# Kernel tuning notes

Hardware: AMD Instinct MI355X
Metric: run time of the kernel (lower is better)

The kernel has to match this reference:

```python
import jax, jax.numpy as jnp
import numpy as np

HID, SD, EXP, DTR = 1024, 16, 2048, 64
B_, T_ = 4, 2048


def setup_inputs() -> dict:
    key = jax.random.key(0)
    ks = jax.random.split(key, 9)
    def rn(k, shape, s=0.02):
        return jax.random.normal(k, shape, jnp.float32) * s
    return {
        "x": jax.random.normal(ks[0], (B_, T_, HID), jnp.float32),
        "ln_g": jnp.ones((HID,), jnp.float32),
        "ln_b": jnp.zeros((HID,), jnp.float32),
        "W_in": rn(ks[1], (HID, 2 * EXP)),
        "b_in": jnp.zeros((2 * EXP,), jnp.float32),
        "W_del": rn(ks[2], (EXP, DTR)),
        "b_del": jnp.zeros((DTR,), jnp.float32),
        "W_dt": rn(ks[3], (DTR, EXP)),
        "b_dt": jnp.zeros((EXP,), jnp.float32),
        "W_B": rn(ks[4], (EXP, SD)),
        "b_B": jnp.zeros((SD,), jnp.float32),
        "W_C": rn(ks[5], (EXP, SD)),
        "b_C": jnp.zeros((SD,), jnp.float32),
        "A_log": -jnp.exp(0.1 * jax.random.normal(ks[6], (EXP, SD), jnp.float32)),
        "Dp": jnp.zeros((EXP,), jnp.float32),
        "W_out": rn(ks[7], (EXP, HID)),
        "b_out": jnp.zeros((HID,), jnp.float32),
    }


def _layernorm(x, g, b, eps=1e-5):
    m = jnp.mean(x, axis=-1, keepdims=True)
    v = jnp.var(x, axis=-1, keepdims=True)
    return (x - m) * jax.lax.rsqrt(v + eps) * g + b


def _selective_scan(u, delta, A, Bm, Cm):
    # u, delta: (B,T,E); Bm, Cm: (B,T,Sd); A: (E,Sd)
    def step(h, inp):
        u_t, d_t, B_t, C_t = inp  # (B,E),(B,E),(B,Sd),(B,Sd)
        A_disc = jnp.exp(d_t[..., None] * A[None])          # (B,E,Sd)
        h = A_disc * h + d_t[..., None] * B_t[:, None, :] * u_t[..., None]
        y_t = jnp.einsum("bs,bds->bd", C_t, h)
        return h, y_t
    h0 = jnp.zeros((u.shape[0], u.shape[2], A.shape[1]), u.dtype)
    xs = (u.transpose(1, 0, 2), delta.transpose(1, 0, 2),
          Bm.transpose(1, 0, 2), Cm.transpose(1, 0, 2))
    _, ys = jax.lax.scan(step, h0, xs)  # ys: (T,B,E)
    return ys.transpose(1, 0, 2)


def reference(x, ln_g, ln_b, W_in, b_in, W_del, b_del, W_dt, b_dt,
              W_B, b_B, W_C, b_C, A_log, Dp, W_out, b_out):
    res = x
    xn = _layernorm(x, ln_g, ln_b)
    xp = xn @ W_in + b_in                 # (B,T,2E)
    u, gate = jnp.split(xp, 2, axis=-1)   # each (B,T,E)
    u = jax.nn.silu(u)
    delta = jax.nn.softplus((u @ W_del + b_del) @ W_dt + b_dt)  # (B,T,E)
    Bm = u @ W_B + b_B                    # (B,T,Sd)
    Cm = u @ W_C + b_C                    # (B,T,Sd)
    A = -jnp.exp(A_log)                   # (E,Sd)
    y = _selective_scan(u, delta, A, Bm, Cm)
    y = y + u * Dp
    y = y * jax.nn.silu(gate)
    return y @ W_out + b_out + res
```

## Files before the change

kernel.cpp:

```cpp
#include <hip/hip_runtime.h>

#define HIDN 1024
#define EXPN 2048
#define SDIM 16
#define DTRN 64
#define BBN  4
#define TTN  2048
#define MMN  (BBN*TTN)
#define NCHUNK 32
#define CLEN (TTN/NCHUNK)
#define KSPL 8
#define KCH  (EXPN/KSPL)

typedef unsigned short u16;
typedef __bf16 bf16x8 __attribute__((ext_vector_type(8)));
typedef float f32x4 __attribute__((ext_vector_type(4)));

static __device__ __forceinline__ float b2f(u16 u) {
    union { unsigned int i; float f; } cv; cv.i = ((unsigned int)u) << 16; return cv.f;
}
static __device__ __forceinline__ u16 f2b(float f) {
    union { float f; unsigned int i; } cv; cv.f = f;
    unsigned int x = cv.i;
    return (u16)((x + 0x7fffu + ((x >> 16) & 1u)) >> 16);
}
static __device__ __forceinline__ float fexp2(float x) {
    return __builtin_amdgcn_exp2f(x);
}
static __device__ __forceinline__ float fsilu(float v) {
    return v / (1.f + fexp2(-1.44269504088896f * v));
}
template<int L> static __device__ __forceinline__ void waitcnt_vm() {
    if constexpr (L == 0) asm volatile("s_waitcnt vmcnt(0)" ::: "memory");
    else if constexpr (L == 3) asm volatile("s_waitcnt vmcnt(3)" ::: "memory");
    else if constexpr (L == 4) asm volatile("s_waitcnt vmcnt(4)" ::: "memory");
}

static __device__ __forceinline__
void tr_tile(const float* __restrict__ W, u16* __restrict__ Wt,
             int K, int N, int bk, int bn, float (*t)[65]) {
    const int r0 = threadIdx.x >> 4, c0 = (threadIdx.x & 15) << 2;
    #pragma unroll
    for (int i = 0; i < 4; ++i) {
        float4 v = *(const float4*)(W + (size_t)(bk + r0 + i * 16) * N + bn + c0);
        t[r0 + i * 16][c0 + 0] = v.x; t[r0 + i * 16][c0 + 1] = v.y;
        t[r0 + i * 16][c0 + 2] = v.z; t[r0 + i * 16][c0 + 3] = v.w;
    }
    __syncthreads();
    #pragma unroll
    for (int i = 0; i < 4; ++i) {
        const int n = r0 + i * 16;
        ushort4 o;
        o.x = f2b(t[c0 + 0][n]); o.y = f2b(t[c0 + 1][n]);
        o.z = f2b(t[c0 + 2][n]); o.w = f2b(t[c0 + 3][n]);
        *(ushort4*)(Wt + (size_t)(bn + n) * K + bk + c0) = o;
    }
}

__global__ __launch_bounds__(256)
void k_prep(const float* __restrict__ x, const float* __restrict__ ln_g,
            const float* __restrict__ ln_b,
            const float* __restrict__ W_in, const float* __restrict__ W_out,
            const float* __restrict__ W_dt, const float* __restrict__ W_del,
            const float* __restrict__ W_B, const float* __restrict__ W_C,
            const float* __restrict__ A_log,
            u16* __restrict__ xn,
            u16* __restrict__ Wt_in, u16* __restrict__ Wt_out,
            u16* __restrict__ Wdt_t, u16* __restrict__ Wcat,
            float* __restrict__ A2) {
    __shared__ float t[64][65];
    __shared__ float as[4], bs[4];
    int blk = blockIdx.x;
    if (blk < MMN) {
        const int row = blk, tid = threadIdx.x;
        const float4 xv = ((const float4*)(x + (size_t)row * HIDN))[tid];
        float s  = xv.x + xv.y + xv.z + xv.w;
        float ss = fmaf(xv.x, xv.x, fmaf(xv.y, xv.y, fmaf(xv.z, xv.z, xv.w * xv.w)));
        #pragma unroll
        for (int o = 32; o > 0; o >>= 1) { s += __shfl_down(s, o); ss += __shfl_down(ss, o); }
        const int wid = tid >> 6, lane = tid & 63;
        if (lane == 0) { as[wid] = s; bs[wid] = ss; }
        __syncthreads();
        const float S  = as[0] + as[1] + as[2] + as[3];
        const float SS = bs[0] + bs[1] + bs[2] + bs[3];
        const float mean = S * (1.f / HIDN);
        const float var  = SS * (1.f / HIDN) - mean * mean;
        const float r = rsqrtf(var + 1e-5f);
        const float4 gv = ((const float4*)ln_g)[tid];
        const float4 bv = ((const float4*)ln_b)[tid];
        ushort4 o;
        o.x = f2b((xv.x - mean) * r * gv.x + bv.x);
        o.y = f2b((xv.y - mean) * r * gv.y + bv.y);
        o.z = f2b((xv.z - mean) * r * gv.z + bv.z);
        o.w = f2b((xv.w - mean) * r * gv.w + bv.w);
        ((ushort4*)(xn + (size_t)row * HIDN))[tid] = o;
        return;
    }
    blk -= MMN;
    if (blk < 1024) {
        tr_tile(W_in, Wt_in, HIDN, 2 * EXPN, (blk >> 6) << 6, (blk & 63) << 6, t);
        return;
    }
    blk -= 1024;
    if (blk < 512) {
        tr_tile(W_out, Wt_out, EXPN, HIDN, (blk >> 4) << 6, (blk & 15) << 6, t);
        return;
    }
    blk -= 512;
    if (blk < 32) {
        tr_tile(W_dt, Wdt_t, DTRN, EXPN, 0, blk << 6, t);
        return;
    }
    blk -= 32;
    if (blk < 768) {
        const int i = blk * 256 + threadIdx.x;
        const int n = i >> 11, k = i & 2047;
        float v;
        if (n < 64)      v = W_del[(size_t)k * DTRN + n];
        else if (n < 80) v = W_B[(size_t)k * SDIM + (n - 64)];
        else             v = W_C[(size_t)k * SDIM + (n - 80)];
        Wcat[i] = f2b(v);
        return;
    }
    blk -= 768;
    {
        const int i = blk * 256 + threadIdx.x;
        A2[i] = -__expf(A_log[i]) * 1.44269504088896340736f;
    }
}

#define MEPI_SPLIT_SILU 0
#define MEPI_OUT        1
#define MEPI_SP         2

template<int BN>
static __device__ __forceinline__
void stage256(const u16* __restrict__ A, const u16* __restrict__ Bt,
              u16 (*seg)[8192], int brow, int bcol, int K, int k0,
              int srow, int scol, int tid) {
    #pragma unroll
    for (int h = 0; h < 2; ++h) {
        const u16* sa = A + (size_t)(brow + h * 128 + srow) * K + k0 + scol;
        __builtin_amdgcn_global_load_lds(
            (const __attribute__((address_space(1))) void*)sa,
            (__attribute__((address_space(3))) void*)&seg[h][tid * 8], 16, 0, 0);
    }
    #pragma unroll
    for (int h = 0; h < BN / 128; ++h) {
        const u16* sb = Bt + (size_t)(bcol + h * 128 + srow) * K + k0 + scol;
        __builtin_amdgcn_global_load_lds(
            (const __attribute__((address_space(1))) void*)sb,
            (__attribute__((address_space(3))) void*)&seg[2 + h][tid * 8], 16, 0, 0);
    }
}

template<int BN, int EPI>
__global__ __launch_bounds__(1024)
void mgemm256(const u16* __restrict__ A, const u16* __restrict__ Bt,
              const float* __restrict__ bias, void* __restrict__ O0,
              void* __restrict__ O1, const float* __restrict__ res,
              int N, int K) {
    constexpr int NSEG = 2 + BN / 128;
    constexpr int L    = NSEG;
    constexpr int NF   = BN / 64 / 4 * 4 / 4;
    constexpr int NFRag = BN / 64;
    __shared__ u16 lds[2][NSEG][8192];
    const int tid  = threadIdx.x;
    const int lane = tid & 63, wid = tid >> 6;
    const int wm = wid >> 2, wn = wid & 3;
    const int r  = lane & 15, kh = lane >> 4;
    const int brow = blockIdx.y * 256, bcol = blockIdx.x * BN;

    int srow, scol;
    {
        const int q = tid;
        const int sub = q >> 6, qi = q & 63;
        const int qis = qi ^ (((qi >> 5) & 1) << 1);
        srow = (sub >> 1) * 16 + (qi >> 2);
        scol = ((sub & 1) << 5) + (qis & 3) * 8;
    }
    const int swz_kh = kh ^ (((r >> 3) & 1) << 1);
    const int rbase  = r * 32 + swz_kh * 8;
    const int am = wm & 1;

    f32x4 acc[4][NFRag];
    #pragma unroll
    for (int i = 0; i < 4; ++i)
        #pragma unroll
        for (int n = 0; n < NFRag; ++n) acc[i][n] = (f32x4){0.f, 0.f, 0.f, 0.f};

    const int NT = K >> 6;
    stage256<BN>(A, Bt, lds[0], brow, bcol, K, 0, srow, scol, tid);
    if (NT > 1) {
        stage256<BN>(A, Bt, lds[1], brow, bcol, K, 64, srow, scol, tid);
        waitcnt_vm<L>();
    } else {
        waitcnt_vm<0>();
    }
    __builtin_amdgcn_s_barrier();
    asm volatile("" ::: "memory");

    for (int kt = 0; kt < NT; ++kt) {
        const u16* segA = lds[kt & 1][wm >> 1];
        #pragma unroll
        for (int kk = 0; kk < 2; ++kk) {
            bf16x8 a[4], b[NFRag];
            #pragma unroll
            for (int mf = 0; mf < 4; ++mf)
                a[mf] = *(const bf16x8*)&segA[((am * 4 + mf) * 2 + kk) * 512 + rbase];
            #pragma unroll
            for (int nf = 0; nf < NFRag; ++nf) {
                const int nb = wn * NFRag + nf;
                const u16* segB = lds[kt & 1][2 + (nb >> 3)];
                b[nf] = *(const bf16x8*)&segB[(((nb & 7)) * 2 + kk) * 512 + rbase];
            }
            __builtin_amdgcn_s_setprio(1);
            #pragma unroll
            for (int mf = 0; mf < 4; ++mf)
                #pragma unroll
                for (int nf = 0; nf < NFRag; ++nf)
                    acc[mf][nf] = __builtin_amdgcn_mfma_f32_16x16x32_bf16(a[mf], b[nf], acc[mf][nf], 0, 0, 0);
            __builtin_amdgcn_s_setprio(0);
        }
        __builtin_amdgcn_s_barrier(); asm volatile("" ::: "memory");
        if (kt + 2 < NT) {
            stage256<BN>(A, Bt, lds[kt & 1], brow, bcol, K, (kt + 2) * 64, srow, scol, tid);
            waitcnt_vm<L>();
        } else {
            waitcnt_vm<0>();
        }
        __builtin_amdgcn_s_barrier(); asm volatile("" ::: "memory");
    }

    const int orow = brow + wm * 64 + kh * 4;
    const int ocol = bcol + wn * (BN / 4) + r;
    if constexpr (EPI == MEPI_SPLIT_SILU) {
        u16* dst; int cb;
        if (bcol < EXPN) { dst = (u16*)O0; cb = ocol; }
        else             { dst = (u16*)O1; cb = ocol - EXPN; }
        #pragma unroll
        for (int Mf = 0; Mf < 4; ++Mf)
            #pragma unroll
            for (int Nf = 0; Nf < NFRag; ++Nf)
                #pragma unroll
                for (int j = 0; j < 4; ++j) {
                    const int row = orow + Mf * 16 + j;
                    const int col = ocol + Nf * 16;
                    float v = acc[Mf][Nf][j] + bias[col];
                    dst[(size_t)row * EXPN + cb + Nf * 16] = f2b(fsilu(v));
                }
    } else if constexpr (EPI == MEPI_SP) {
        u16* o = (u16*)O0;
        #pragma unroll
        for (int Mf = 0; Mf < 4; ++Mf)
            #pragma unroll
            for (int Nf = 0; Nf < NFRag; ++Nf)
                #pragma unroll
                for (int j = 0; j < 4; ++j) {
                    const int row = orow + Mf * 16 + j;
                    const int col = ocol + Nf * 16;
                    float v = acc[Mf][Nf][j] + bias[col];
                    float sp = (v > 20.f) ? v
                             : 0.69314718056f * __builtin_amdgcn_logf(
                                   1.f + fexp2(1.44269504089f * v));
                    o[(size_t)row * N + col] = f2b(sp);
                }
    } else {
        float* o = (float*)O0;
        #pragma unroll
        for (int Mf = 0; Mf < 4; ++Mf)
            #pragma unroll
            for (int Nf = 0; Nf < NFRag; ++Nf)
                #pragma unroll
                for (int j = 0; j < 4; ++j) {
                    const int row = orow + Mf * 16 + j;
                    const int col = ocol + Nf * 16;
                    o[(size_t)row * N + col] = acc[Mf][Nf][j] + bias[col] + res[(size_t)row * N + col];
                }
    }
}

__global__ __launch_bounds__(256)
void k_proj(const u16* __restrict__ A, const u16* __restrict__ Wcat,
            float* __restrict__ Ppart) {
    __shared__ u16 As[128 * 32];
    __shared__ u16 Bs[96 * 32];
    const int tid  = threadIdx.x;
    const int wave = tid >> 6, lane = tid & 63;
    const int brow = blockIdx.y * 128;
    const int ks   = blockIdx.x;
    const int r = lane & 15, kh = lane >> 4;

    f32x4 acc[2][6];
    #pragma unroll
    for (int m = 0; m < 2; m++)
        #pragma unroll
        for (int n = 0; n < 6; n++) acc[m][n] = (f32x4){0.f, 0.f, 0.f, 0.f};

    const u16* ga0 = A + (size_t)(brow +      (tid >> 2)) * EXPN + ks * KCH + (tid & 3) * 8;
    const u16* ga1 = A + (size_t)(brow + 64 + (tid >> 2)) * EXPN + ks * KCH + (tid & 3) * 8;
    const u16* gb0 = Wcat + (size_t)(tid >> 2) * EXPN + ks * KCH + (tid & 3) * 8;
    const u16* gb1 = Wcat + (size_t)(64 + (tid >> 2)) * EXPN + ks * KCH + (tid & 3) * 8;
    u16* lA0 = As + (wave * 64) * 8;
    u16* lA1 = As + (256 + wave * 64) * 8;
    u16* lB0 = Bs + (wave * 64) * 8;
    u16* lB1 = Bs + (256 + wave * 64) * 8;

    for (int k0 = 0; k0 < KCH; k0 += 32) {
        __syncthreads();
        __builtin_amdgcn_global_load_lds((const __attribute__((address_space(1))) void*)(ga0 + k0),
                                         (__attribute__((address_space(3))) void*)lA0, 16, 0, 0);
        __builtin_amdgcn_global_load_lds((const __attribute__((address_space(1))) void*)(ga1 + k0),
                                         (__attribute__((address_space(3))) void*)lA1, 16, 0, 0);
        __builtin_amdgcn_global_load_lds((const __attribute__((address_space(1))) void*)(gb0 + k0),
                                         (__attribute__((address_space(3))) void*)lB0, 16, 0, 0);
        if (tid < 128)
            __builtin_amdgcn_global_load_lds((const __attribute__((address_space(1))) void*)(gb1 + k0),
                                             (__attribute__((address_space(3))) void*)lB1, 16, 0, 0);
        __syncthreads();
        bf16x8 af[2], bfr[6];
        #pragma unroll
        for (int mf = 0; mf < 2; ++mf)
            af[mf] = *(const bf16x8*)(As + ((wave * 32 + mf * 16 + r) * 32 + kh * 8));
        #pragma unroll
        for (int nf = 0; nf < 6; ++nf)
            bfr[nf] = *(const bf16x8*)(Bs + ((nf * 16 + r) * 32 + kh * 8));
        #pragma unroll
        for (int mf = 0; mf < 2; ++mf)
            #pragma unroll
            for (int nf = 0; nf < 6; ++nf)
                acc[mf][nf] = __builtin_amdgcn_mfma_f32_16x16x32_bf16(af[mf], bfr[nf], acc[mf][nf], 0, 0, 0);
    }
    const int orow = brow + wave * 32 + kh * 4;
    #pragma unroll
    for (int mf = 0; mf < 2; ++mf)
        #pragma unroll
        for (int nf = 0; nf < 6; ++nf)
            #pragma unroll
            for (int j = 0; j < 4; ++j)
                Ppart[((size_t)ks * MMN + orow + mf * 16 + j) * 96 + nf * 16 + r] = acc[mf][nf][j];
}

__global__ __launch_bounds__(192)
void k_red(const float* __restrict__ Ppart, const float* __restrict__ b_del,
           const float* __restrict__ b_B, const float* __restrict__ b_C,
           u16* __restrict__ t1b, float* __restrict__ Bm, float* __restrict__ Cm) {
    const int tid = threadIdx.x;
    const int ri  = tid / 96, col = tid - ri * 96;
    const int row = blockIdx.x * 2 + ri;
    float s = 0.f;
    #pragma unroll
    for (int ks = 0; ks < KSPL; ++ks)
        s += Ppart[((size_t)ks * MMN + row) * 96 + col];
    if (col < 64)      t1b[(size_t)row * DTRN + col] = f2b(s + b_del[col]);
    else if (col < 80) Bm[(size_t)row * SDIM + col - 64] = s + b_B[col - 64];
    else               Cm[(size_t)row * SDIM + col - 80] = s + b_C[col - 80];
}

__global__ __launch_bounds__(256)
void k_scan1(const u16* __restrict__ ub, const u16* __restrict__ db,
             const float* __restrict__ Bm, const float* __restrict__ A2,
             float* __restrict__ hend, float* __restrict__ Pp) {
    const int e = blockIdx.x * 256 + threadIdx.x;
    const int c = blockIdx.y, b = blockIdx.z;
    float a2[SDIM], h[SDIM];
    {
        const float4* ap = (const float4*)(A2 + (size_t)e * SDIM);
        float4 v0 = ap[0], v1 = ap[1], v2 = ap[2], v3 = ap[3];
        a2[0]=v0.x; a2[1]=v0.y; a2[2]=v0.z; a2[3]=v0.w;
        a2[4]=v1.x; a2[5]=v1.y; a2[6]=v1.z; a2[7]=v1.w;
        a2[8]=v2.x; a2[9]=v2.y; a2[10]=v2.z; a2[11]=v2.w;
        a2[12]=v3.x; a2[13]=v3.y; a2[14]=v3.z; a2[15]=v3.w;
    }
    #pragma unroll
    for (int s = 0; s < SDIM; s++) h[s] = 0.f;
    float sumd = 0.f;
    const int t0 = c * CLEN;
    size_t rb = ((size_t)b * TTN + t0) * EXPN + e;
    size_t bb_ = ((size_t)b * TTN + t0) * SDIM;
    for (int tt = 0; tt < CLEN; ++tt) {
        const float d  = b2f(db[rb]);
        const float uv = b2f(ub[rb]);
        const float4* bp = (const float4*)(Bm + bb_);
        float4 b0 = bp[0], b1 = bp[1], b2v = bp[2], b3 = bp[3];
        float bv[SDIM] = { b0.x,b0.y,b0.z,b0.w, b1.x,b1.y,b1.z,b1.w,
                           b2v.x,b2v.y,b2v.z,b2v.w, b3.x,b3.y,b3.z,b3.w };
        const float du = d * uv;
        sumd += d;
        #pragma unroll
        for (int s = 0; s < SDIM; ++s) {
            float ad = fexp2(d * a2[s]);
            h[s] = fmaf(ad, h[s], du * bv[s]);
        }
        rb += EXPN; bb_ += SDIM;
    }
    size_t ob = ((size_t)(b * NCHUNK + c) * SDIM) * EXPN + e;
    #pragma unroll
    for (int s = 0; s < SDIM; ++s) {
        hend[ob + (size_t)s * EXPN] = h[s];
        Pp  [ob + (size_t)s * EXPN] = fexp2(a2[s] * sumd);
    }
}

__global__ __launch_bounds__(256)
void k_fix(const float* __restrict__ hend, const float* __restrict__ Pp,
           float* __restrict__ hinit) {
    const int i = blockIdx.x * 256 + threadIdx.x;
    const int b = blockIdx.y;
    float hi = 0.f;
    size_t base = ((size_t)b * NCHUNK) * SDIM * EXPN + i;
    for (int cc = 0; cc < NCHUNK; ++cc) {
        size_t idx = base + (size_t)cc * SDIM * EXPN;
        hinit[idx] = hi;
        hi = fmaf(Pp[idx], hi, hend[idx]);
    }
}

__global__ __launch_bounds__(256)
void k_scan2(const u16* __restrict__ ub, const u16* __restrict__ db,
             const u16* __restrict__ sgb, const float* __restrict__ Bm,
             const float* __restrict__ Cm, const float* __restrict__ A2,
             const float* __restrict__ hinit, const float* __restrict__ Dp,
             u16* __restrict__ yb) {
    const int e = blockIdx.x * 256 + threadIdx.x;
    const int c = blockIdx.y, b = blockIdx.z;
    float a2[SDIM], h[SDIM];
    {
        const float4* ap = (const float4*)(A2 + (size_t)e * SDIM);
        float4 v0 = ap[0], v1 = ap[1], v2 = ap[2], v3 = ap[3];
        a2[0]=v0.x; a2[1]=v0.y; a2[2]=v0.z; a2[3]=v0.w;
        a2[4]=v1.x; a2[5]=v1.y; a2[6]=v1.z; a2[7]=v1.w;
        a2[8]=v2.x; a2[9]=v2.y; a2[10]=v2.z; a2[11]=v2.w;
        a2[12]=v3.x; a2[13]=v3.y; a2[14]=v3.z; a2[15]=v3.w;
    }
    {
        size_t hb = ((size_t)(b * NCHUNK + c) * SDIM) * EXPN + e;
        #pragma unroll
        for (int s = 0; s < SDIM; s++) h[s] = hinit[hb + (size_t)s * EXPN];
    }
    const float dpe = Dp[e];
    const int t0 = c * CLEN;
    size_t rb = ((size_t)b * TTN + t0) * EXPN + e;
    size_t bb_ = ((size_t)b * TTN + t0) * SDIM;
    for (int tt = 0; tt < CLEN; ++tt) {
        const float d   = b2f(db[rb]);
        const float uv  = b2f(ub[rb]);
        const float sgv = b2f(sgb[rb]);
        const float4* bp = (const float4*)(Bm + bb_);
        const float4* cp = (const float4*)(Cm + bb_);
        float4 b0 = bp[0], b1 = bp[1], b2v = bp[2], b3 = bp[3];
        float4 c0 = cp[0], c1 = cp[1], c2v = cp[2], c3 = cp[3];
        float bv[SDIM] = { b0.x,b0.y,b0.z,b0.w, b1.x,b1.y,b1.z,b1.w,
                           b2v.x,b2v.y,b2v.z,b2v.w, b3.x,b3.y,b3.z,b3.w };
        float cv[SDIM] = { c0.x,c0.y,c0.z,c0.w, c1.x,c1.y,c1.z,c1.w,
                           c2v.x,c2v.y,c2v.z,c2v.w, c3.x,c3.y,c3.z,c3.w };
        const float du = d * uv;
        float yt = 0.f;
        #pragma unroll
        for (int s = 0; s < SDIM; ++s) {
            float ad = fexp2(d * a2[s]);
            h[s] = fmaf(ad, h[s], du * bv[s]);
            yt = fmaf(cv[s], h[s], yt);
        }
        yb[rb] = f2b(fmaf(uv, dpe, yt) * sgv);
        rb += EXPN; bb_ += SDIM;
    }
}

extern "C" void kernel_launch(void* const* d_in, const int* in_sizes, int n_in,
                              void* d_out, int out_size, void* d_ws, size_t ws_size,
                              hipStream_t stream) {
    const float* x     = (const float*)d_in[0];
    const float* ln_g  = (const float*)d_in[1];
    const float* ln_b  = (const float*)d_in[2];
    const float* W_in  = (const float*)d_in[3];
    const float* b_in  = (const float*)d_in[4];
    const float* W_del = (const float*)d_in[5];
    const float* b_del = (const float*)d_in[6];
    const float* W_dt  = (const float*)d_in[7];
    const float* b_dt  = (const float*)d_in[8];
    const float* W_B   = (const float*)d_in[9];
    const float* b_B   = (const float*)d_in[10];
    const float* W_C   = (const float*)d_in[11];
    const float* b_C   = (const float*)d_in[12];
    const float* A_log = (const float*)d_in[13];
    const float* Dp    = (const float*)d_in[14];
    const float* W_out = (const float*)d_in[15];
    const float* b_out = (const float*)d_in[16];
    float* out = (float*)d_out;

    char* p = (char*)d_ws;
    auto alloc = [&](size_t bytes) {
        char* r = p; p += (bytes + 255) & ~(size_t)255; return (void*)r;
    };
    u16* xn   = (u16*)alloc((size_t)MMN * HIDN * 2);
    u16* u    = (u16*)alloc((size_t)MMN * EXPN * 2);
    u16* sg   = (u16*)alloc((size_t)MMN * EXPN * 2);
    u16* dl   = (u16*)alloc((size_t)MMN * EXPN * 2);
    u16* y    = (u16*)alloc((size_t)MMN * EXPN * 2);
    u16* t1b  = (u16*)alloc((size_t)MMN * DTRN * 2);
    float* Bm = (float*)alloc((size_t)MMN * SDIM * 4);
    float* Cm = (float*)alloc((size_t)MMN * SDIM * 4);
    float* A2 = (float*)alloc((size_t)EXPN * SDIM * 4);
    u16* Wt_in  = (u16*)alloc((size_t)(2 * EXPN) * HIDN * 2);
    u16* Wt_out = (u16*)alloc((size_t)HIDN * EXPN * 2);
    u16* Wcat   = (u16*)alloc((size_t)96 * EXPN * 2);
    u16* Wdt_t  = (u16*)alloc((size_t)EXPN * DTRN * 2);
    const size_t hsz = (size_t)BBN * NCHUNK * EXPN * SDIM * 4;
    float* hend  = (float*)alloc(hsz);
    float* Pp    = (float*)alloc(hsz);
    float* hinit = (float*)alloc(hsz);
    float* Ppart = hend;

    k_prep<<<dim3(MMN + 1024 + 512 + 32 + 768 + 128), 256, 0, stream>>>(
        x, ln_g, ln_b, W_in, W_out, W_dt, W_del, W_B, W_C, A_log,
        xn, Wt_in, Wt_out, Wdt_t, Wcat, A2);

    mgemm256<256, MEPI_SPLIT_SILU><<<dim3(2 * EXPN / 256, MMN / 256), 1024, 0, stream>>>(
        xn, Wt_in, b_in, u, sg, nullptr, 2 * EXPN, HIDN);
    k_proj<<<dim3(KSPL, MMN / 128), 256, 0, stream>>>(u, Wcat, Ppart);
    k_red<<<dim3(MMN / 2), 192, 0, stream>>>(Ppart, b_del, b_B, b_C, t1b, Bm, Cm);
    mgemm256<128, MEPI_SP><<<dim3(EXPN / 128, MMN / 256), 1024, 0, stream>>>(
        t1b, Wdt_t, b_dt, dl, nullptr, nullptr, EXPN, DTRN);
    k_scan1<<<dim3(EXPN / 256, NCHUNK, BBN), 256, 0, stream>>>(u, dl, Bm, A2, hend, Pp);
    k_fix<<<dim3(SDIM * EXPN / 256, BBN), 256, 0, stream>>>(hend, Pp, hinit);
    k_scan2<<<dim3(EXPN / 256, NCHUNK, BBN), 256, 0, stream>>>(u, dl, sg, Bm, Cm, A2, hinit, Dp, y);
    mgemm256<128, MEPI_OUT><<<dim3(HIDN / 128, MMN / 256), 1024, 0, stream>>>(
        y, Wt_out, b_out, out, nullptr, x, HIDN, EXPN);
}
```

Before: 294.2 us.

## Double scan chunks, store chunk states in bf16, pack scan math

Doubles the number of scan chunks so the two scan passes expose more parallelism over shorter sequential runs. Chunk end states, decay products and initial states now go to memory as bf16 in an element-major layout, written and read as 16-byte vectors, which cuts inter-pass traffic. The inner recurrence is written with two-wide float vectors so the compiler can emit packed FMA/mul instructions. The bf16 storage of carried states adds rounding error to the recurrence, and the extra chunks lengthen the serial k_fix pass.

```diff
diff --git a/kernel.cpp b/kernel.cpp
--- a/kernel.cpp
+++ b/kernel.cpp
@@ -7,7 +7,7 @@
 #define BBN  4
 #define TTN  2048
 #define MMN  (BBN*TTN)
-#define NCHUNK 32
+#define NCHUNK 64
 #define CLEN (TTN/NCHUNK)
 #define KSPL 8
 #define KCH  (EXPN/KSPL)
@@ -15,6 +15,7 @@
 typedef unsigned short u16;
 typedef __bf16 bf16x8 __attribute__((ext_vector_type(8)));
 typedef float f32x4 __attribute__((ext_vector_type(4)));
+typedef float f32x2v __attribute__((ext_vector_type(2)));
 
 static __device__ __forceinline__ float b2f(u16 u) {
     union { unsigned int i; float f; } cv; cv.i = ((unsigned int)u) << 16; return cv.f;
@@ -162,7 +163,6 @@
               int N, int K) {
     constexpr int NSEG = 2 + BN / 128;
     constexpr int L    = NSEG;
-    constexpr int NF   = BN / 64 / 4 * 4 / 4;
     constexpr int NFRag = BN / 64;
     __shared__ u16 lds[2][NSEG][8192];
     const int tid  = threadIdx.x;
@@ -360,20 +360,21 @@
 __global__ __launch_bounds__(256)
 void k_scan1(const u16* __restrict__ ub, const u16* __restrict__ db,
              const float* __restrict__ Bm, const float* __restrict__ A2,
-             float* __restrict__ hend, float* __restrict__ Pp) {
+             u16* __restrict__ hend, u16* __restrict__ Pp) {
     const int e = blockIdx.x * 256 + threadIdx.x;
     const int c = blockIdx.y, b = blockIdx.z;
-    float a2[SDIM], h[SDIM];
+    f32x2v a2p[8], hp[8];
     {
         const float4* ap = (const float4*)(A2 + (size_t)e * SDIM);
-        float4 v0 = ap[0], v1 = ap[1], v2 = ap[2], v3 = ap[3];
-        a2[0]=v0.x; a2[1]=v0.y; a2[2]=v0.z; a2[3]=v0.w;
-        a2[4]=v1.x; a2[5]=v1.y; a2[6]=v1.z; a2[7]=v1.w;
-        a2[8]=v2.x; a2[9]=v2.y; a2[10]=v2.z; a2[11]=v2.w;
-        a2[12]=v3.x; a2[13]=v3.y; a2[14]=v3.z; a2[15]=v3.w;
-    }
-    #pragma unroll
-    for (int s = 0; s < SDIM; s++) h[s] = 0.f;
+        #pragma unroll
+        for (int q = 0; q < 4; ++q) {
+            float4 v = ap[q];
+            a2p[2*q]   = (f32x2v){v.x, v.y};
+            a2p[2*q+1] = (f32x2v){v.z, v.w};
+        }
+    }
+    #pragma unroll
+    for (int i = 0; i < 8; ++i) hp[i] = (f32x2v){0.f, 0.f};
     float sumd = 0.f;
     const int t0 = c * CLEN;
     size_t rb = ((size_t)b * TTN + t0) * EXPN + e;
@@ -382,37 +383,49 @@
         const float d  = b2f(db[rb]);
         const float uv = b2f(ub[rb]);
         const float4* bp = (const float4*)(Bm + bb_);
-        float4 b0 = bp[0], b1 = bp[1], b2v = bp[2], b3 = bp[3];
-        float bv[SDIM] = { b0.x,b0.y,b0.z,b0.w, b1.x,b1.y,b1.z,b1.w,
-                           b2v.x,b2v.y,b2v.z,b2v.w, b3.x,b3.y,b3.z,b3.w };
+        f32x2v bvp[8];
+        #pragma unroll
+        for (int q = 0; q < 4; ++q) {
+            float4 v = bp[q];
+            bvp[2*q]   = (f32x2v){v.x, v.y};
+            bvp[2*q+1] = (f32x2v){v.z, v.w};
+        }
         const float du = d * uv;
         sumd += d;
         #pragma unroll
-        for (int s = 0; s < SDIM; ++s) {
-            float ad = fexp2(d * a2[s]);
-            h[s] = fmaf(ad, h[s], du * bv[s]);
+        for (int i = 0; i < 8; ++i) {
+            f32x2v arg = a2p[i] * d;
+            f32x2v ad; ad.x = fexp2(arg.x); ad.y = fexp2(arg.y);
+            hp[i] = ad * hp[i] + bvp[i] * du;
         }
         rb += EXPN; bb_ += SDIM;
     }
-    size_t ob = ((size_t)(b * NCHUNK + c) * SDIM) * EXPN + e;
-    #pragma unroll
-    for (int s = 0; s < SDIM; ++s) {
-        hend[ob + (size_t)s * EXPN] = h[s];
-        Pp  [ob + (size_t)s * EXPN] = fexp2(a2[s] * sumd);
-    }
+    const size_t base = ((size_t)((b * NCHUNK + c)) * EXPN + e) * 16;
+    union { u16 s[16]; uint4 v[2]; } he, pv;
+    #pragma unroll
+    for (int i = 0; i < 8; ++i) {
+        he.s[2*i]   = f2b(hp[i].x);
+        he.s[2*i+1] = f2b(hp[i].y);
+        pv.s[2*i]   = f2b(fexp2(a2p[i].x * sumd));
+        pv.s[2*i+1] = f2b(fexp2(a2p[i].y * sumd));
+    }
+    *(uint4*)(hend + base)     = he.v[0];
+    *(uint4*)(hend + base + 8) = he.v[1];
+    *(uint4*)(Pp + base)       = pv.v[0];
+    *(uint4*)(Pp + base + 8)   = pv.v[1];
 }
 
 __global__ __launch_bounds__(256)
-void k_fix(const float* __restrict__ hend, const float* __restrict__ Pp,
-           float* __restrict__ hinit) {
+void k_fix(const u16* __restrict__ hend, const u16* __restrict__ Pp,
+           u16* __restrict__ hinit) {
     const int i = blockIdx.x * 256 + threadIdx.x;
     const int b = blockIdx.y;
     float hi = 0.f;
-    size_t base = ((size_t)b * NCHUNK) * SDIM * EXPN + i;
+    size_t idx = (size_t)b * NCHUNK * (EXPN * 16) + i;
     for (int cc = 0; cc < NCHUNK; ++cc) {
-        size_t idx = base + (size_t)cc * SDIM * EXPN;
-        hinit[idx] = hi;
-        hi = fmaf(Pp[idx], hi, hend[idx]);
+        hinit[idx] = f2b(hi);
+        hi = fmaf(b2f(Pp[idx]), hi, b2f(hend[idx]));
+        idx += EXPN * 16;
     }
 }
 
@@ -420,23 +433,28 @@
 void k_scan2(const u16* __restrict__ ub, const u16* __restrict__ db,
              const u16* __restrict__ sgb, const float* __restrict__ Bm,
              const float* __restrict__ Cm, const float* __restrict__ A2,
-             const float* __restrict__ hinit, const float* __restrict__ Dp,
+             const u16* __restrict__ hinit, const float* __restrict__ Dp,
              u16* __restrict__ yb) {
     const int e = blockIdx.x * 256 + threadIdx.x;
     const int c = blockIdx.y, b = blockIdx.z;
-    float a2[SDIM], h[SDIM];
+    f32x2v a2p[8], hp[8];
     {
         const float4* ap = (const float4*)(A2 + (size_t)e * SDIM);
-        float4 v0 = ap[0], v1 = ap[1], v2 = ap[2], v3 = ap[3];
-        a2[0]=v0.x; a2[1]=v0.y; a2[2]=v0.z; a2[3]=v0.w;
-        a2[4]=v1.x; a2[5]=v1.y; a2[6]=v1.z; a2[7]=v1.w;
-        a2[8]=v2.x; a2[9]=v2.y; a2[10]=v2.z; a2[11]=v2.w;
-        a2[12]=v3.x; a2[13]=v3.y; a2[14]=v3.z; a2[15]=v3.w;
+        #pragma unroll
+        for (int q = 0; q < 4; ++q) {
+            float4 v = ap[q];
+            a2p[2*q]   = (f32x2v){v.x, v.y};
+            a2p[2*q+1] = (f32x2v){v.z, v.w};
+        }
     }
     {
-        size_t hb = ((size_t)(b * NCHUNK + c) * SDIM) * EXPN + e;
-        #pragma unroll
-        for (int s = 0; s < SDIM; s++) h[s] = hinit[hb + (size_t)s * EXPN];
+        const size_t base = ((size_t)((b * NCHUNK + c)) * EXPN + e) * 16;
+        union { u16 s[16]; uint4 v[2]; } hi;
+        hi.v[0] = *(const uint4*)(hinit + base);
+        hi.v[1] = *(const uint4*)(hinit + base + 8);
+        #pragma unroll
+        for (int i = 0; i < 8; ++i)
+            hp[i] = (f32x2v){b2f(hi.s[2*i]), b2f(hi.s[2*i+1])};
     }
     const float dpe = Dp[e];
     const int t0 = c * CLEN;
@@ -448,20 +466,26 @@
         const float sgv = b2f(sgb[rb]);
         const float4* bp = (const float4*)(Bm + bb_);
         const float4* cp = (const float4*)(Cm + bb_);
-        float4 b0 = bp[0], b1 = bp[1], b2v = bp[2], b3 = bp[3];
-        float4 c0 = cp[0], c1 = cp[1], c2v = cp[2], c3 = cp[3];
-        float bv[SDIM] = { b0.x,b0.y,b0.z,b0.w, b1.x,b1.y,b1.z,b1.w,
-                           b2v.x,b2v.y,b2v.z,b2v.w, b3.x,b3.y,b3.z,b3.w };
-        float cv[SDIM] = { c0.x,c0.y,c0.z,c0.w, c1.x,c1.y,c1.z,c1.w,
-                           c2v.x,c2v.y,c2v.z,c2v.w, c3.x,c3.y,c3.z,c3.w };
+        f32x2v bvp[8], cvp[8];
+        #pragma unroll
+        for (int q = 0; q < 4; ++q) {
+            float4 v = bp[q];
+            bvp[2*q]   = (f32x2v){v.x, v.y};
+            bvp[2*q+1] = (f32x2v){v.z, v.w};
+            float4 w = cp[q];
+            cvp[2*q]   = (f32x2v){w.x, w.y};
+            cvp[2*q+1] = (f32x2v){w.z, w.w};
+        }
         const float du = d * uv;
-        float yt = 0.f;
-        #pragma unroll
-        for (int s = 0; s < SDIM; ++s) {
-            float ad = fexp2(d * a2[s]);
-            h[s] = fmaf(ad, h[s], du * bv[s]);
-            yt = fmaf(cv[s], h[s], yt);
-        }
+        f32x2v ytp = (f32x2v){0.f, 0.f};
+        #pragma unroll
+        for (int i = 0; i < 8; ++i) {
+            f32x2v arg = a2p[i] * d;
+            f32x2v ad; ad.x = fexp2(arg.x); ad.y = fexp2(arg.y);
+            hp[i] = ad * hp[i] + bvp[i] * du;
+            ytp = ytp + cvp[i] * hp[i];
+        }
+        const float yt = ytp.x + ytp.y;
         yb[rb] = f2b(fmaf(uv, dpe, yt) * sgv);
         rb += EXPN; bb_ += SDIM;
     }
@@ -506,11 +530,11 @@
     u16* Wt_out = (u16*)alloc((size_t)HIDN * EXPN * 2);
     u16* Wcat   = (u16*)alloc((size_t)96 * EXPN * 2);
     u16* Wdt_t  = (u16*)alloc((size_t)EXPN * DTRN * 2);
-    const size_t hsz = (size_t)BBN * NCHUNK * EXPN * SDIM * 4;
-    float* hend  = (float*)alloc(hsz);
-    float* Pp    = (float*)alloc(hsz);
-    float* hinit = (float*)alloc(hsz);
-    float* Ppart = hend;
+    const size_t hsz = (size_t)BBN * NCHUNK * EXPN * SDIM * 2;
+    u16* hend  = (u16*)alloc(hsz);
+    u16* Pp    = (u16*)alloc(hsz);
+    u16* hinit = (u16*)alloc(hsz);
+    float* Ppart = (float*)hend;
 
     k_prep<<<dim3(MMN + 1024 + 512 + 32 + 768 + 128), 256, 0, stream>>>(
         x, ln_g, ln_b, W_in, W_out, W_dt, W_del, W_B, W_C, A_log,
@@ -523,7 +547,7 @@
     mgemm256<128, MEPI_SP><<<dim3(EXPN / 128, MMN / 256), 1024, 0, stream>>>(
         t1b, Wdt_t, b_dt, dl, nullptr, nullptr, EXPN, DTRN);
     k_scan1<<<dim3(EXPN / 256, NCHUNK, BBN), 256, 0, stream>>>(u, dl, Bm, A2, hend, Pp);
-    k_fix<<<dim3(SDIM * EXPN / 256, BBN), 256, 0, stream>>>(hend, Pp, hinit);
+    k_fix<<<dim3(EXPN * SDIM / 256, BBN), 256, 0, stream>>>(hend, Pp, hinit);
     k_scan2<<<dim3(EXPN / 256, NCHUNK, BBN), 256, 0, stream>>>(u, dl, sg, Bm, Cm, A2, hinit, Dp, y);
     mgemm256<128, MEPI_OUT><<<dim3(HIDN / 128, MMN / 256), 1024, 0, stream>>>(
         y, Wt_out, b_out, out, nullptr, x, HIDN, EXPN);
```

Result: faster. 283.4 us (-3.7%).
